# Kernel tuning notes

Hardware: AMD Instinct MI355X
Metric: run time of the kernel (lower is better)

Reference implementation:

```python
import jax, jax.numpy as jnp
import numpy as np

B, T, C = 4, 2048, 1024
NH = 16
HD = C // NH


def setup_inputs() -> dict:
    key = jax.random.key(0)
    ks = jax.random.split(key, 5)
    s = 1.0 / np.sqrt(C)
    return {
        "x": jax.random.normal(ks[0], (B, T, C), dtype=jnp.float32),
        "W_qkv": jax.random.normal(ks[1], (C, 3 * C), dtype=jnp.float32) * s,
        "b_qkv": jnp.zeros((3 * C,), dtype=jnp.float32),
        "W_out": jax.random.normal(ks[2], (C, C), dtype=jnp.float32) * s,
        "b_out": jnp.zeros((C,), dtype=jnp.float32),
    }


def reference(x, W_qkv, b_qkv, W_out, b_out):
    Bx, Tx, Cx = x.shape
    qkv = x @ W_qkv + b_qkv                      # [B,T,3C]
    q, k, v = jnp.split(qkv, 3, axis=2)
    # [B,T,C] -> [B,NH,T,HD]
    q = q.reshape(Bx, Tx, NH, HD).transpose(0, 2, 1, 3)
    k = k.reshape(Bx, Tx, NH, HD).transpose(0, 2, 1, 3)
    v = v.reshape(Bx, Tx, NH, HD).transpose(0, 2, 1, 3)
    scale = 1.0 / np.sqrt(HD).astype(np.float32)
    attn = jnp.einsum('bhqd,bhkd->bhqk', q, k) * scale  # [B,NH,T,T]
    causal = jnp.tril(jnp.ones((Tx, Tx), dtype=bool))
    attn = jnp.where(causal[None, None], attn, jnp.float32(-jnp.inf))
    attn = jax.nn.softmax(attn, axis=-1)
    out = jnp.einsum('bhqk,bhkd->bhqd', attn, v)        # [B,NH,T,HD]
    out = out.transpose(0, 2, 1, 3).reshape(Bx, Tx, Cx)
    y = out @ W_out + b_out
    return (y, k, v)
```

## Files before the change

### kernel.cpp

```cpp
#include <hip/hip_runtime.h>
#include <cstdint>
#include <cstddef>

typedef __bf16 bf16x8 __attribute__((ext_vector_type(8)));
typedef __bf16 bf16x4 __attribute__((ext_vector_type(4)));
typedef float  f32x4  __attribute__((ext_vector_type(4)));

#define MFMA16(a, b, c) __builtin_amdgcn_mfma_f32_16x16x32_bf16((a), (b), (c), 0, 0, 0)

#define GLL16(gsrc, ldst)                                                              \
  __builtin_amdgcn_global_load_lds((__attribute__((address_space(1))) void*)(gsrc),    \
                                   (__attribute__((address_space(3))) void*)(ldst),    \
                                   16, 0, 0)

#define QSCALE 0.1803368801111204f


__global__ __launch_bounds__(256)
void cvt_f32_bf16(const float* __restrict__ in, __bf16* __restrict__ out, int n4)
{
    int i = blockIdx.x * 256 + threadIdx.x;
    if (i < n4) {
        float4 v = ((const float4*)in)[i];
        bf16x4 o;
        o[0] = (__bf16)v.x; o[1] = (__bf16)v.y; o[2] = (__bf16)v.z; o[3] = (__bf16)v.w;
        ((bf16x4*)out)[i] = o;
    }
}

__global__ __launch_bounds__(256)
void transpose_cvt(const float* __restrict__ in, __bf16* __restrict__ out, int K, int N)
{
    __shared__ __bf16 tile[32][33];
    const int n0 = blockIdx.x * 32, k0 = blockIdx.y * 32;
    const int tx = threadIdx.x, ty = threadIdx.y;
    #pragma unroll
    for (int i = 0; i < 4; ++i)
        tile[ty + i * 8][tx] = (__bf16)in[(size_t)(k0 + ty + i * 8) * N + n0 + tx];
    __syncthreads();
    #pragma unroll
    for (int i = 0; i < 4; ++i)
        out[(size_t)(n0 + ty + i * 8) * K + k0 + tx] = tile[tx][ty + i * 8];
}


__global__ __launch_bounds__(256)
void vtrans(const float* __restrict__ vout, __bf16* __restrict__ vwst)
{
    const int bh = blockIdx.y;
    const int t0 = blockIdx.x * 64;
    const int tid = threadIdx.x;

    __shared__ __bf16 VT[64][68];

    const int tr = tid >> 4;
    const int dc = (tid & 15) * 4;

    float4 vals[4];
    #pragma unroll
    for (int i = 0; i < 4; ++i)
        vals[i] = *(const float4*)&vout[((size_t)bh * 2048 + t0 + tr + 16 * i) * 64 + dc];

    #pragma unroll
    for (int j = 0; j < 4; ++j) {
        bf16x4 pk;
        pk[0] = (__bf16)(&vals[0].x)[j];
        pk[1] = (__bf16)(&vals[1].x)[j];
        pk[2] = (__bf16)(&vals[2].x)[j];
        pk[3] = (__bf16)(&vals[3].x)[j];
        *(bf16x4*)&VT[dc + j][4 * tr] = pk;
    }
    __syncthreads();

    #pragma unroll
    for (int k = 0; k < 2; ++k) {
        const int c = tid + 256 * k;
        const int d = c >> 3, off = (c & 7) * 8;
        bf16x8 v = *(const bf16x8*)&VT[d][off];
        *(bf16x8*)&vwst[((size_t)bh * 64 + d) * 2048 + t0 + off] = v;
    }
}


__global__ __launch_bounds__(256)
void gemm_qkv(const __bf16* __restrict__ A, const __bf16* __restrict__ Bt,
              const float* __restrict__ bias,
              __bf16* __restrict__ qws, float* __restrict__ kout, float* __restrict__ vout,
              __bf16* __restrict__ kws)
{
    constexpr int K = 1024;
    const int m0 = blockIdx.y * 128, n0 = blockIdx.x * 128;
    const int tid = threadIdx.x;
    const int wave = tid >> 6, lane = tid & 63;
    const int quad = lane >> 4, lr = lane & 15;
    const int wrow = (wave & 1) * 64, wcol = (wave >> 1) * 64;

    __shared__ __bf16 As[128 * 32];
    __shared__ __bf16 Bs[128 * 32];

    f32x4 acc[4][4];
    #pragma unroll
    for (int mi = 0; mi < 4; ++mi)
      #pragma unroll
      for (int ni = 0; ni < 4; ++ni)
        #pragma unroll
        for (int c = 0; c < 4; ++c) acc[mi][ni][c] = 0.f;

    const int u0 = tid, u1 = tid + 256;
    const int cg0 = ((u0 & 3) ^ ((u0 >> 3) & 3)) * 8;
    const int cg1 = ((u1 & 3) ^ ((u1 >> 3) & 3)) * 8;
    const __bf16* ga0 = A  + (size_t)(m0 + (u0 >> 2)) * K + cg0;
    const __bf16* ga1 = A  + (size_t)(m0 + (u1 >> 2)) * K + cg1;
    const __bf16* gb0 = Bt + (size_t)(n0 + (u0 >> 2)) * K + cg0;
    const __bf16* gb1 = Bt + (size_t)(n0 + (u1 >> 2)) * K + cg1;
    __bf16* la0 = As + u0 * 8;
    __bf16* la1 = As + u1 * 8;
    __bf16* lb0 = Bs + u0 * 8;
    __bf16* lb1 = Bs + u1 * 8;

    const int sw = (quad ^ ((lr >> 1) & 3)) * 8;

    for (int kt = 0; kt < K; kt += 32) {
        __syncthreads();
        GLL16(ga0 + kt, la0);
        GLL16(ga1 + kt, la1);
        GLL16(gb0 + kt, lb0);
        GLL16(gb1 + kt, lb1);
        __syncthreads();
        bf16x8 af[4], bfv[4];
        #pragma unroll
        for (int mi = 0; mi < 4; ++mi)
            af[mi] = *(const bf16x8*)&As[(wrow + mi * 16 + lr) * 32 + sw];
        #pragma unroll
        for (int ni = 0; ni < 4; ++ni)
            bfv[ni] = *(const bf16x8*)&Bs[(wcol + ni * 16 + lr) * 32 + sw];
        #pragma unroll
        for (int mi = 0; mi < 4; ++mi)
          #pragma unroll
          for (int ni = 0; ni < 4; ++ni)
            acc[mi][ni] = MFMA16(af[mi], bfv[ni], acc[mi][ni]);
    }

    const int sec = n0 >> 10;
    #pragma unroll
    for (int ni = 0; ni < 4; ++ni) {
        const int gn = n0 + wcol + ni * 16 + lr;
        const float bv = bias[gn];
        const int cn = gn & 1023, hh = cn >> 6, dd = cn & 63;
        #pragma unroll
        for (int mi = 0; mi < 4; ++mi) {
            const int gm0 = m0 + wrow + mi * 16 + quad * 4;
            const int b = gm0 >> 11, t0 = gm0 & 2047;
            const size_t tb = ((size_t)b * 16 + hh) * 2048;
            if (sec == 0) {
                #pragma unroll
                for (int r = 0; r < 4; ++r)
                    qws[(tb + t0 + r) * 64 + dd] = (__bf16)((acc[mi][ni][r] + bv) * QSCALE);
            } else if (sec == 1) {
                #pragma unroll
                for (int r = 0; r < 4; ++r) {
                    const float val = acc[mi][ni][r] + bv;
                    kout[(tb + t0 + r) * 64 + dd] = val;
                    kws [(tb + t0 + r) * 64 + dd] = (__bf16)val;
                }
            } else {
                #pragma unroll
                for (int r = 0; r < 4; ++r)
                    vout[(tb + t0 + r) * 64 + dd] = acc[mi][ni][r] + bv;
            }
        }
    }
}


__global__ __launch_bounds__(256)
void gemm_out(const __bf16* __restrict__ A, const __bf16* __restrict__ Bt,
              const float* __restrict__ bias, float* __restrict__ y)
{
    constexpr int K = 1024;
    const int m0 = blockIdx.y * 64, n0 = blockIdx.x * 128;
    const int tid = threadIdx.x;
    const int wave = tid >> 6, lane = tid & 63;
    const int quad = lane >> 4, lr = lane & 15;
    const int wrow = (wave & 1) * 32, wcol = (wave >> 1) * 64;

    __shared__ __bf16 As[64 * 32];
    __shared__ __bf16 Bs[128 * 32];

    f32x4 acc[2][4];
    #pragma unroll
    for (int mi = 0; mi < 2; ++mi)
      #pragma unroll
      for (int ni = 0; ni < 4; ++ni)
        #pragma unroll
        for (int c = 0; c < 4; ++c) acc[mi][ni][c] = 0.f;

    const int ua = tid, u0 = tid, u1 = tid + 256;
    const int cga = ((ua & 3) ^ ((ua >> 3) & 3)) * 8;
    const int cg0 = ((u0 & 3) ^ ((u0 >> 3) & 3)) * 8;
    const int cg1 = ((u1 & 3) ^ ((u1 >> 3) & 3)) * 8;
    const __bf16* ga  = A  + (size_t)(m0 + (ua >> 2)) * K + cga;
    const __bf16* gb0 = Bt + (size_t)(n0 + (u0 >> 2)) * K + cg0;
    const __bf16* gb1 = Bt + (size_t)(n0 + (u1 >> 2)) * K + cg1;
    __bf16* la  = As + ua * 8;
    __bf16* lb0 = Bs + u0 * 8;
    __bf16* lb1 = Bs + u1 * 8;

    const int sw = (quad ^ ((lr >> 1) & 3)) * 8;

    for (int kt = 0; kt < K; kt += 32) {
        __syncthreads();
        GLL16(ga + kt, la);
        GLL16(gb0 + kt, lb0);
        GLL16(gb1 + kt, lb1);
        __syncthreads();
        bf16x8 af[2], bfv[4];
        #pragma unroll
        for (int mi = 0; mi < 2; ++mi)
            af[mi] = *(const bf16x8*)&As[(wrow + mi * 16 + lr) * 32 + sw];
        #pragma unroll
        for (int ni = 0; ni < 4; ++ni)
            bfv[ni] = *(const bf16x8*)&Bs[(wcol + ni * 16 + lr) * 32 + sw];
        #pragma unroll
        for (int mi = 0; mi < 2; ++mi)
          #pragma unroll
          for (int ni = 0; ni < 4; ++ni)
            acc[mi][ni] = MFMA16(af[mi], bfv[ni], acc[mi][ni]);
    }

    #pragma unroll
    for (int ni = 0; ni < 4; ++ni) {
        const int gn = n0 + wcol + ni * 16 + lr;
        const float bv = bias[gn];
        #pragma unroll
        for (int mi = 0; mi < 2; ++mi) {
            #pragma unroll
            for (int r = 0; r < 4; ++r) {
                const int gm = m0 + wrow + mi * 16 + quad * 4 + r;
                y[(size_t)gm * 1024 + gn] = acc[mi][ni][r] + bv;
            }
        }
    }
}


__global__ __launch_bounds__(256, 2)
void attn_fused(const __bf16* __restrict__ qws, const __bf16* __restrict__ kws,
                const __bf16* __restrict__ vwst, __bf16* __restrict__ attnws)
{
    const int bh = blockIdx.x;
    const int tid = threadIdx.x;
    const int wave = tid >> 6, lane = tid & 63;
    const int quad = lane >> 4, lr = lane & 15;

    const int jqp[2] = { (int)blockIdx.y, 15 - (int)blockIdx.y };
    const int ntp[2] = { 2 * (jqp[0] + 1), 2 * (jqp[1] + 1) };
    const int nt0 = ntp[0];
    const int ntot = 34;

    __shared__ __bf16 Ks [3][2][64][32];
    __shared__ __bf16 Vts[3][2][64][32];
    __shared__ __bf16 Ps [4][32][72];

    const int srow = tid >> 2;
    const int scg  = ((tid & 3) ^ ((tid >> 3) & 3)) * 8;
    const __bf16* kb = kws  + ((size_t)bh * 2048 + srow) * 64 + scg;
    const __bf16* vb = vwst + ((size_t)bh * 64 + srow) * 2048 + scg;
    char* lk = (char*)Ks  + tid * 16;
    char* lv = (char*)Vts + tid * 16;

    const int sw = (quad ^ ((lr >> 1) & 3)) * 8;

    bf16x8 ones;
    #pragma unroll
    for (int j = 0; j < 8; ++j) ones[j] = (__bf16)1.0f;

    bf16x8 aq[2][2][2];
    #pragma unroll
    for (int h = 0; h < 2; ++h)
      #pragma unroll
      for (int mi = 0; mi < 2; ++mi) {
        const __bf16* qb = qws + ((size_t)bh * 2048 + jqp[h] * 128 + wave * 32 + mi * 16 + lr) * 64 + quad * 8;
        aq[h][mi][0] = *(const bf16x8*)qb;
        aq[h][mi][1] = *(const bf16x8*)(qb + 32);
      }

#define PREFETCH(j, buf)                                                \
    do {                                                                \
        GLL16(kb + (size_t)(j) * 4096,      lk + (buf) * 8192);         \
        GLL16(kb + (size_t)(j) * 4096 + 32, lk + (buf) * 8192 + 4096);  \
        GLL16(vb + (j) * 64,                lv + (buf) * 8192);         \
        GLL16(vb + (j) * 64 + 32,           lv + (buf) * 8192 + 4096);  \
    } while (0)

    PREFETCH(0, 0);
    PREFETCH(1, 1);

    bf16x4 oreg[2][2][4];

    int pos = 0;
    for (int h = 0; h < 2; ++h) {
        const int jq = jqp[h];
        const int NT = ntp[h];

        f32x4 o_acc[2][4], l_acc[2];
        #pragma unroll
        for (int mi = 0; mi < 2; ++mi) {
            #pragma unroll
            for (int r = 0; r < 4; ++r) l_acc[mi][r] = 0.f;
            #pragma unroll
            for (int n = 0; n < 4; ++n)
                #pragma unroll
                for (int r = 0; r < 4; ++r) o_acc[mi][n][r] = 0.f;
        }

        for (int jt = 0; jt < NT; ++jt, ++pos) {
            const int cur = pos % 3;
            if (pos + 1 < ntot) {
                asm volatile("s_waitcnt vmcnt(4)" ::: "memory");
            } else {
                asm volatile("s_waitcnt vmcnt(0)" ::: "memory");
            }
            asm volatile("s_waitcnt lgkmcnt(0)" ::: "memory");
            asm volatile("s_barrier" ::: "memory");
            if (pos + 2 < ntot) {
                const int p2 = pos + 2;
                const int nj = (p2 < nt0) ? p2 : p2 - nt0;
                PREFETCH(nj, p2 % 3);
            }

            const bool lastTile = (jt == NT - 1);
            if (!(lastTile && wave < 2)) {
                bf16x8 bk[4][2];
                #pragma unroll
                for (int ni = 0; ni < 4; ++ni) {
                    bk[ni][0] = *(const bf16x8*)&Ks[cur][0][ni * 16 + lr][sw];
                    bk[ni][1] = *(const bf16x8*)&Ks[cur][1][ni * 16 + lr][sw];
                }
                f32x4 sacc[2][4];
                #pragma unroll
                for (int mi = 0; mi < 2; ++mi)
                  #pragma unroll
                  for (int ni = 0; ni < 4; ++ni)
                    #pragma unroll
                    for (int c = 0; c < 4; ++c) sacc[mi][ni][c] = -12.f;
                #pragma unroll
                for (int ni = 0; ni < 4; ++ni)
                  #pragma unroll
                  for (int mi = 0; mi < 2; ++mi) {
                    sacc[mi][ni] = MFMA16(aq[h][mi][0], bk[ni][0], sacc[mi][ni]);
                    sacc[mi][ni] = MFMA16(aq[h][mi][1], bk[ni][1], sacc[mi][ni]);
                  }

                const bool needMask = (jt == NT - 2 && wave < 2) || (lastTile && wave >= 2);
                if (needMask) {
                    const int c0 = jt * 64 + lr;
                    #pragma unroll
                    for (int mi = 0; mi < 2; ++mi) {
                        const int t0 = jq * 128 + wave * 32 + mi * 16 + quad * 4;
                        #pragma unroll
                        for (int ni = 0; ni < 4; ++ni)
                          #pragma unroll
                          for (int r = 0; r < 4; ++r)
                            if (c0 + ni * 16 > t0 + r) sacc[mi][ni][r] = -1e30f;
                    }
                }

                #pragma unroll
                for (int mi = 0; mi < 2; ++mi)
                  #pragma unroll
                  for (int r = 0; r < 4; ++r) {
                    bf16x4 pp;
                    #pragma unroll
                    for (int ni = 0; ni < 4; ++ni)
                        pp[ni] = (__bf16)__builtin_amdgcn_exp2f(sacc[mi][ni][r]);
                    *(bf16x4*)&Ps[wave][mi * 16 + quad * 4 + r][4 * lr] = pp;
                  }

                asm volatile("s_waitcnt lgkmcnt(0)" ::: "memory");

                bf16x8 bv[4][2];
                #pragma unroll
                for (int n = 0; n < 4; ++n) {
                    bv[n][0] = *(const bf16x8*)&Vts[cur][0][n * 16 + lr][sw];
                    bv[n][1] = *(const bf16x8*)&Vts[cur][1][n * 16 + lr][sw];
                }
                #pragma unroll
                for (int mi = 0; mi < 2; ++mi) {
                    bf16x8 ap0 = *(const bf16x8*)&Ps[wave][mi * 16 + lr][quad * 8];
                    bf16x8 ap1 = *(const bf16x8*)&Ps[wave][mi * 16 + lr][32 + quad * 8];
                    l_acc[mi] = MFMA16(ap0, ones, l_acc[mi]);
                    l_acc[mi] = MFMA16(ap1, ones, l_acc[mi]);
                    #pragma unroll
                    for (int n = 0; n < 4; ++n) {
                        o_acc[mi][n] = MFMA16(ap0, bv[n][0], o_acc[mi][n]);
                        o_acc[mi][n] = MFMA16(ap1, bv[n][1], o_acc[mi][n]);
                    }
                }
            }
        }

        #pragma unroll
        for (int mi = 0; mi < 2; ++mi)
          #pragma unroll
          for (int r = 0; r < 4; ++r) {
            const float inv = 1.f / l_acc[mi][r];
            #pragma unroll
            for (int n = 0; n < 4; ++n)
                oreg[h][mi][n][r] = (__bf16)(o_acc[mi][n][r] * inv);
          }
    }

    const int b = bh >> 4, h16 = bh & 15;
    #pragma unroll
    for (int h = 0; h < 2; ++h)
      #pragma unroll
      for (int mi = 0; mi < 2; ++mi)
        #pragma unroll
        for (int r = 0; r < 4; ++r) {
            const int t = jqp[h] * 128 + wave * 32 + mi * 16 + quad * 4 + r;
            #pragma unroll
            for (int n = 0; n < 4; ++n)
                attnws[(((size_t)b * 2048 + t) * 16 + h16) * 64 + n * 16 + lr] =
                    oreg[h][mi][n][r];
        }
#undef PREFETCH
}


extern "C" void kernel_launch(void* const* d_in, const int* in_sizes, int n_in,
                              void* d_out, int out_size, void* d_ws, size_t ws_size,
                              hipStream_t stream)
{
    (void)in_sizes; (void)n_in; (void)out_size; (void)ws_size;

    const float* x    = (const float*)d_in[0];
    const float* Wqkv = (const float*)d_in[1];
    const float* bqkv = (const float*)d_in[2];
    const float* Wout = (const float*)d_in[3];
    const float* bout = (const float*)d_in[4];

    float* y    = (float*)d_out;
    float* kout = y + 8388608;
    float* vout = kout + 8388608;

    char* ws = (char*)d_ws;
    __bf16* xb    = (__bf16*)(ws);
    __bf16* wqkvt = (__bf16*)(ws + (16u << 20));
    __bf16* woutt = (__bf16*)(ws + (22u << 20));
    __bf16* qws   = (__bf16*)(ws + (24u << 20));
    __bf16* kws   = (__bf16*)(ws + (40u << 20));
    __bf16* vwst  = (__bf16*)(ws + (56u << 20));
    __bf16* attnw = (__bf16*)(ws + (72u << 20));

    cvt_f32_bf16<<<8192, 256, 0, stream>>>(x, xb, 2097152);
    transpose_cvt<<<dim3(96, 32), dim3(32, 8), 0, stream>>>(Wqkv, wqkvt, 1024, 3072);
    transpose_cvt<<<dim3(32, 32), dim3(32, 8), 0, stream>>>(Wout, woutt, 1024, 1024);
    gemm_qkv<<<dim3(24, 64), 256, 0, stream>>>(xb, wqkvt, bqkv, qws, kout, vout, kws);
    vtrans<<<dim3(32, 64), 256, 0, stream>>>(vout, vwst);
    attn_fused<<<dim3(64, 8), 256, 0, stream>>>(qws, kws, vwst, attnw);
    gemm_out<<<dim3(8, 128), 256, 0, stream>>>(attnw, woutt, bout, y);
}
```

Measured before the change: 305.6 us.

## Rewrite QKV GEMM with 256x192 tiles, 8 waves, and double-buffered LDS pipeline

The QKV projection GEMM moves from 128x128 tiles with 4 waves to 256x192 tiles with 8 waves. A double-buffered 64-wide K pipeline issues global-to-LDS loads interleaved with MFMA phases, using explicit waitcnt/barrier and setprio around MFMA bursts. This targets the exposed load latency and per-step double sync of the old loop, and raises data reuse per tile. In exchange it uses more LDS and registers and is sensitive to barrier ordering. It also computes the section per column, since a 192-wide tile no longer aligns to the 1024 boundaries.

Result: no change. 304.5 us (-0.4%).

```diff
diff --git a/kernel.cpp b/kernel.cpp
--- a/kernel.cpp
+++ b/kernel.cpp
@@ -82,73 +82,149 @@
 }
 
 
-__global__ __launch_bounds__(256)
+__global__ __launch_bounds__(512, 2)
 void gemm_qkv(const __bf16* __restrict__ A, const __bf16* __restrict__ Bt,
               const float* __restrict__ bias,
               __bf16* __restrict__ qws, float* __restrict__ kout, float* __restrict__ vout,
               __bf16* __restrict__ kws)
 {
     constexpr int K = 1024;
-    const int m0 = blockIdx.y * 128, n0 = blockIdx.x * 128;
+    const int m0 = blockIdx.y * 256, n0 = blockIdx.x * 192;
     const int tid = threadIdx.x;
     const int wave = tid >> 6, lane = tid & 63;
     const int quad = lane >> 4, lr = lane & 15;
-    const int wrow = (wave & 1) * 64, wcol = (wave >> 1) * 64;
-
-    __shared__ __bf16 As[128 * 32];
-    __shared__ __bf16 Bs[128 * 32];
-
-    f32x4 acc[4][4];
-    #pragma unroll
-    for (int mi = 0; mi < 4; ++mi)
+    const int wm = wave & 1, wn = wave >> 1;
+    const int wrow = wm * 128, wcol = wn * 48;
+
+    __shared__ __bf16 As[2][2][256][32];
+    __shared__ __bf16 Bs[2][2][192][32];
+
+    f32x4 acc[8][3];
+    #pragma unroll
+    for (int mi = 0; mi < 8; ++mi)
       #pragma unroll
-      for (int ni = 0; ni < 4; ++ni)
+      for (int ni = 0; ni < 3; ++ni)
         #pragma unroll
         for (int c = 0; c < 4; ++c) acc[mi][ni][c] = 0.f;
 
-    const int u0 = tid, u1 = tid + 256;
-    const int cg0 = ((u0 & 3) ^ ((u0 >> 3) & 3)) * 8;
-    const int cg1 = ((u1 & 3) ^ ((u1 >> 3) & 3)) * 8;
-    const __bf16* ga0 = A  + (size_t)(m0 + (u0 >> 2)) * K + cg0;
-    const __bf16* ga1 = A  + (size_t)(m0 + (u1 >> 2)) * K + cg1;
-    const __bf16* gb0 = Bt + (size_t)(n0 + (u0 >> 2)) * K + cg0;
-    const __bf16* gb1 = Bt + (size_t)(n0 + (u1 >> 2)) * K + cg1;
-    __bf16* la0 = As + u0 * 8;
-    __bf16* la1 = As + u1 * 8;
-    __bf16* lb0 = Bs + u0 * 8;
-    __bf16* lb1 = Bs + u1 * 8;
+    const __bf16* gA[4];
+    #pragma unroll
+    for (int l = 0; l < 4; ++l) {
+        const int u = tid + 512 * l;
+        const int kc = u >> 10;
+        const int row = (u >> 2) & 255;
+        const int cg = ((u & 3) ^ ((u >> 3) & 3)) * 8;
+        gA[l] = A + (size_t)(m0 + row) * K + kc * 32 + cg;
+    }
+    const __bf16* gB[3];
+    #pragma unroll
+    for (int l = 0; l < 3; ++l) {
+        const int u = tid + 512 * l;
+        const int kc = (u >= 768);
+        const int row = (u - kc * 768) >> 2;
+        const int cg = ((u & 3) ^ ((u >> 3) & 3)) * 8;
+        gB[l] = Bt + (size_t)(n0 + row) * K + kc * 32 + cg;
+    }
+    char* lA = (char*)As + tid * 16;
+    char* lB = (char*)Bs + tid * 16;
 
     const int sw = (quad ^ ((lr >> 1) & 3)) * 8;
 
-    for (int kt = 0; kt < K; kt += 32) {
-        __syncthreads();
-        GLL16(ga0 + kt, la0);
-        GLL16(ga1 + kt, la1);
-        GLL16(gb0 + kt, lb0);
-        GLL16(gb1 + kt, lb1);
-        __syncthreads();
-        bf16x8 af[4], bfv[4];
-        #pragma unroll
-        for (int mi = 0; mi < 4; ++mi)
-            af[mi] = *(const bf16x8*)&As[(wrow + mi * 16 + lr) * 32 + sw];
-        #pragma unroll
-        for (int ni = 0; ni < 4; ++ni)
-            bfv[ni] = *(const bf16x8*)&Bs[(wcol + ni * 16 + lr) * 32 + sw];
-        #pragma unroll
-        for (int mi = 0; mi < 4; ++mi)
-          #pragma unroll
-          for (int ni = 0; ni < 4; ++ni)
-            acc[mi][ni] = MFMA16(af[mi], bfv[ni], acc[mi][ni]);
-    }
-
-    const int sec = n0 >> 10;
-    #pragma unroll
-    for (int ni = 0; ni < 4; ++ni) {
+    GLL16(gA[0], lA);
+    GLL16(gA[1], lA + 8192);
+    GLL16(gA[2], lA + 16384);
+    GLL16(gA[3], lA + 24576);
+    GLL16(gB[0], lB);
+    GLL16(gB[1], lB + 8192);
+    GLL16(gB[2], lB + 16384);
+    GLL16(gA[0] + 64, lA + 32768);
+    GLL16(gA[1] + 64, lA + 40960);
+    asm volatile("s_waitcnt vmcnt(2)" ::: "memory");
+    asm volatile("s_barrier" ::: "memory");
+
+    bf16x8 bfv[3];
+
+#define PHASE(buf, kc, mh, ...)                                                    \
+    do {                                                                           \
+        if ((mh) == 0) {                                                           \
+            bfv[0] = *(const bf16x8*)&Bs[buf][kc][wcol      + lr][sw];             \
+            bfv[1] = *(const bf16x8*)&Bs[buf][kc][wcol + 16 + lr][sw];             \
+            bfv[2] = *(const bf16x8*)&Bs[buf][kc][wcol + 32 + lr][sw];             \
+        }                                                                          \
+        bf16x8 af0 = *(const bf16x8*)&As[buf][kc][wrow + (mh)*64      + lr][sw];   \
+        bf16x8 af1 = *(const bf16x8*)&As[buf][kc][wrow + (mh)*64 + 16 + lr][sw];   \
+        bf16x8 af2 = *(const bf16x8*)&As[buf][kc][wrow + (mh)*64 + 32 + lr][sw];   \
+        bf16x8 af3 = *(const bf16x8*)&As[buf][kc][wrow + (mh)*64 + 48 + lr][sw];   \
+        __VA_ARGS__                                                                \
+        asm volatile("s_barrier" ::: "memory");                                    \
+        __builtin_amdgcn_s_setprio(1);                                             \
+        acc[(mh)*4+0][0] = MFMA16(af0, bfv[0], acc[(mh)*4+0][0]);                  \
+        acc[(mh)*4+0][1] = MFMA16(af0, bfv[1], acc[(mh)*4+0][1]);                  \
+        acc[(mh)*4+0][2] = MFMA16(af0, bfv[2], acc[(mh)*4+0][2]);                  \
+        acc[(mh)*4+1][0] = MFMA16(af1, bfv[0], acc[(mh)*4+1][0]);                  \
+        acc[(mh)*4+1][1] = MFMA16(af1, bfv[1], acc[(mh)*4+1][1]);                  \
+        acc[(mh)*4+1][2] = MFMA16(af1, bfv[2], acc[(mh)*4+1][2]);                  \
+        acc[(mh)*4+2][0] = MFMA16(af2, bfv[0], acc[(mh)*4+2][0]);                  \
+        acc[(mh)*4+2][1] = MFMA16(af2, bfv[1], acc[(mh)*4+2][1]);                  \
+        acc[(mh)*4+2][2] = MFMA16(af2, bfv[2], acc[(mh)*4+2][2]);                  \
+        acc[(mh)*4+3][0] = MFMA16(af3, bfv[0], acc[(mh)*4+3][0]);                  \
+        acc[(mh)*4+3][1] = MFMA16(af3, bfv[1], acc[(mh)*4+3][1]);                  \
+        acc[(mh)*4+3][2] = MFMA16(af3, bfv[2], acc[(mh)*4+3][2]);                  \
+        __builtin_amdgcn_s_setprio(0);                                             \
+        asm volatile("s_barrier" ::: "memory");                                    \
+    } while (0)
+
+    for (int it = 0; it < 8; ++it) {
+        const bool more = (it < 7);
+
+        PHASE(0, 0, 0, {
+            GLL16(gA[2] + 64, lA + 16384 + 32768);
+            GLL16(gA[3] + 64, lA + 24576 + 32768);
+            GLL16(gB[0] + 64, lB + 24576);
+            GLL16(gB[1] + 64, lB +  8192 + 24576);
+            GLL16(gB[2] + 64, lB + 16384 + 24576);
+        });
+        PHASE(0, 0, 1, {});
+        PHASE(0, 1, 0, {
+            if (more) { GLL16(gA[0] + 128, lA); GLL16(gA[1] + 128, lA + 8192); }
+        });
+        PHASE(0, 1, 1, {
+            if (more) asm volatile("s_waitcnt vmcnt(2)" ::: "memory");
+            else      asm volatile("s_waitcnt vmcnt(0)" ::: "memory");
+        });
+        PHASE(1, 0, 0, {
+            if (more) {
+                GLL16(gA[2] + 128, lA + 16384);
+                GLL16(gA[3] + 128, lA + 24576);
+                GLL16(gB[0] + 128, lB);
+                GLL16(gB[1] + 128, lB + 8192);
+                GLL16(gB[2] + 128, lB + 16384);
+            }
+        });
+        PHASE(1, 0, 1, {});
+        PHASE(1, 1, 0, {
+            if (more) { GLL16(gA[0] + 192, lA + 32768); GLL16(gA[1] + 192, lA + 40960); }
+        });
+        PHASE(1, 1, 1, {
+            if (more) asm volatile("s_waitcnt vmcnt(2)" ::: "memory");
+            else      asm volatile("s_waitcnt vmcnt(0)" ::: "memory");
+        });
+
+        #pragma unroll
+        for (int l = 0; l < 4; ++l) gA[l] += 128;
+        #pragma unroll
+        for (int l = 0; l < 3; ++l) gB[l] += 128;
+    }
+#undef PHASE
+
+    #pragma unroll
+    for (int ni = 0; ni < 3; ++ni) {
         const int gn = n0 + wcol + ni * 16 + lr;
         const float bv = bias[gn];
+        const int sec = gn >> 10;
         const int cn = gn & 1023, hh = cn >> 6, dd = cn & 63;
         #pragma unroll
-        for (int mi = 0; mi < 4; ++mi) {
+        for (int mi = 0; mi < 8; ++mi) {
             const int gm0 = m0 + wrow + mi * 16 + quad * 4;
             const int b = gm0 >> 11, t0 = gm0 & 2047;
             const size_t tb = ((size_t)b * 16 + hh) * 2048;
@@ -456,7 +532,7 @@
     cvt_f32_bf16<<<8192, 256, 0, stream>>>(x, xb, 2097152);
     transpose_cvt<<<dim3(96, 32), dim3(32, 8), 0, stream>>>(Wqkv, wqkvt, 1024, 3072);
     transpose_cvt<<<dim3(32, 32), dim3(32, 8), 0, stream>>>(Wout, woutt, 1024, 1024);
-    gemm_qkv<<<dim3(24, 64), 256, 0, stream>>>(xb, wqkvt, bqkv, qws, kout, vout, kws);
+    gemm_qkv<<<dim3(16, 32), 512, 0, stream>>>(xb, wqkvt, bqkv, qws, kout, vout, kws);
     vtrans<<<dim3(32, 64), 256, 0, stream>>>(vout, vwst);
     attn_fused<<<dim3(64, 8), 256, 0, stream>>>(qws, kws, vwst, attnw);
     gemm_out<<<dim3(8, 128), 256, 0, stream>>>(attnw, woutt, bout, y);
```
